# Optimization experiments

Hardware: AMD Instinct MI355X
Metric: run time of the kernel (lower is better)

Reference implementation:

```python
import jax, jax.numpy as jnp
import numpy as np

SEQ = 4096
EMB = 1024
OUT = 1024


def setup_inputs() -> dict:
    key = jax.random.key(0)
    k_x, k_q, k_k, k_v = jax.random.split(key, 4)
    scale = 1.0 / np.sqrt(EMB)
    inputs = jax.random.normal(k_x, (SEQ, EMB), dtype=jnp.float32)
    # torch Linear weight is (out_features, in_features); y = x @ W.T
    W_Q = jax.random.normal(k_q, (OUT, EMB), dtype=jnp.float32) * scale
    W_K = jax.random.normal(k_k, (OUT, EMB), dtype=jnp.float32) * scale
    W_V = jax.random.normal(k_v, (OUT, EMB), dtype=jnp.float32) * scale
    return {"inputs": inputs, "W_Q": W_Q, "W_K": W_K, "W_V": W_V}


def reference(inputs, W_Q, W_K, W_V):
    # projections: (S, E) @ (E, D) -> (S, D)
    q = inputs @ W_Q.T
    k = inputs @ W_K.T
    v = inputs @ W_V.T
    d_k = k.shape[-1]
    scores = (q @ k.T) / jnp.sqrt(jnp.asarray(d_k, dtype=q.dtype))  # (S, S)
    weights = jax.nn.softmax(scores, axis=-1)
    return weights @ v  # (S, D)
```

## Files before the change

kernel.cpp:

```cpp
#include <hip/hip_runtime.h>

typedef __bf16 bf16;
typedef __bf16 bf16x4 __attribute__((ext_vector_type(4)));
typedef __bf16 bf16x8 __attribute__((ext_vector_type(8)));
typedef float f32x4 __attribute__((ext_vector_type(4)));

#define SEQ 4096
#define EMB 1024

#define MODE_BF16 0
#define MODE_EXP  1
#define MODE_PART 2

__device__ __forceinline__ void async_copy16(void* lds, const void* g) {
    __builtin_amdgcn_global_load_lds(
        (const __attribute__((address_space(1))) unsigned int*)g,
        (__attribute__((address_space(3))) unsigned int*)lds,
        16, 0, 0);
}

__global__ __launch_bounds__(256) void cvt_f32_bf16(const float* __restrict__ src,
                                                    bf16* __restrict__ dst, int n)
{
    int i = (blockIdx.x * 256 + threadIdx.x) * 4;
    if (i < n) {
        float4 f = *(const float4*)(src + i);
        bf16x4 v = { (bf16)f.x, (bf16)f.y, (bf16)f.z, (bf16)f.w };
        *(bf16x4*)(dst + i) = v;
    }
}

template<int OUT_MODE>
__global__ __launch_bounds__(256) void gemm_bt(const bf16* __restrict__ A,
                                               const bf16* __restrict__ B,
                                               void* __restrict__ Cv,
                                               float* __restrict__ Cpart,
                                               int lda, int ldb, int ldc, int K)
{
    __shared__ __align__(16) bf16 As[128 * 64];
    __shared__ __align__(16) bf16 Bs[128 * 64];

    const int tid  = threadIdx.x;
    const int lane = tid & 63;
    const int wave = tid >> 6;
    const int m0 = blockIdx.y * 128;
    const int n0 = blockIdx.x * 128;
    const size_t koff = (size_t)blockIdx.z * K;

    const int srow = tid >> 3;
    const int spc  = tid & 7;
    const int sl   = (spc - (srow & 7)) & 7;

    const int wm = (wave & 1) << 6;
    const int wn = (wave >> 1) << 6;
    const int fr = lane & 15;
    const int q  = lane >> 4;

    f32x4 acc[4][4];
    for (int i = 0; i < 4; i++)
        for (int j = 0; j < 4; j++)
            acc[i][j] = {0.f, 0.f, 0.f, 0.f};

    const bf16* Ab = A + (size_t)(m0 + srow) * lda + koff + sl * 8;
    const bf16* Bb = B + (size_t)(n0 + srow) * ldb + koff + sl * 8;

    bf16* AsD = &As[srow * 64 + spc * 8];
    bf16* BsD = &Bs[srow * 64 + spc * 8];

    const int pc0 = ((q + fr) & 7) * 8;
    const int pc1 = (((q + fr) & 7) ^ 4) * 8;

    for (int k0 = 0; k0 < K; k0 += 64) {
        __syncthreads();
        for (int t = 0; t < 4; t++) {
            async_copy16(AsD + t * 2048, Ab + k0 + (size_t)(32 * t) * lda);
            async_copy16(BsD + t * 2048, Bb + k0 + (size_t)(32 * t) * ldb);
        }
        __syncthreads();

        bf16x8 af[4], bg[4];
        for (int i = 0; i < 4; i++)
            af[i] = *(const bf16x8*)&As[(wm + i * 16 + fr) * 64 + pc0];
        for (int j = 0; j < 4; j++)
            bg[j] = *(const bf16x8*)&Bs[(wn + j * 16 + fr) * 64 + pc0];
        for (int i = 0; i < 4; i++)
            for (int j = 0; j < 4; j++)
                acc[i][j] = __builtin_amdgcn_mfma_f32_16x16x32_bf16(af[i], bg[j], acc[i][j], 0, 0, 0);
        for (int i = 0; i < 4; i++)
            af[i] = *(const bf16x8*)&As[(wm + i * 16 + fr) * 64 + pc1];
        for (int j = 0; j < 4; j++)
            bg[j] = *(const bf16x8*)&Bs[(wn + j * 16 + fr) * 64 + pc1];
        for (int i = 0; i < 4; i++)
            for (int j = 0; j < 4; j++)
                acc[i][j] = __builtin_amdgcn_mfma_f32_16x16x32_bf16(af[i], bg[j], acc[i][j], 0, 0, 0);
    }

    const int cm = m0 + wm + (q << 2);
    const int cn = n0 + wn + fr;
    if (OUT_MODE == MODE_BF16) {
        bf16* C = (bf16*)Cv;
        for (int i = 0; i < 4; i++)
            for (int j = 0; j < 4; j++)
                for (int r = 0; r < 4; r++)
                    C[(size_t)(cm + i * 16 + r) * ldc + (cn + j * 16)] = (bf16)acc[i][j][r];
    } else if (OUT_MODE == MODE_EXP) {
        bf16* C = (bf16*)Cv;
        for (int i = 0; i < 4; i++)
            for (int j = 0; j < 4; j++)
                for (int r = 0; r < 4; r++)
                    C[(size_t)(cm + i * 16 + r) * ldc + (cn + j * 16)] =
                        (bf16)__expf(acc[i][j][r] * 0.03125f);
    } else {
        float* C = (blockIdx.z == 0) ? (float*)Cv
                                     : Cpart + (size_t)(blockIdx.z - 1) * SEQ * 1024;
        for (int i = 0; i < 4; i++)
            for (int j = 0; j < 4; j++)
                for (int r = 0; r < 4; r++)
                    C[(size_t)(cm + i * 16 + r) * ldc + (cn + j * 16)] = acc[i][j][r];
    }
}

__global__ __launch_bounds__(256) void reduce_norm(const bf16* __restrict__ E,
                                                   const float* __restrict__ p1,
                                                   const float* __restrict__ p2,
                                                   const float* __restrict__ p3,
                                                   float* __restrict__ out)
{
    const int m = blockIdx.x;
    const int tid = threadIdx.x;

    const bf16* er = E + (size_t)m * 4096;
    bf16x8 v0 = *(const bf16x8*)&er[tid * 16];
    bf16x8 v1 = *(const bf16x8*)&er[tid * 16 + 8];
    float s = 0.f;
    for (int i = 0; i < 8; i++) s += (float)v0[i] + (float)v1[i];
    for (int t = 1; t < 64; t <<= 1) s += __shfl_xor(s, t);

    __shared__ float red[4];
    if ((tid & 63) == 0) red[tid >> 6] = s;
    __syncthreads();
    const float inv = 1.f / (red[0] + red[1] + red[2] + red[3]);

    const size_t off = (size_t)m * 1024 + tid * 4;
    float4 a = *(const float4*)(out + off);
    float4 b = *(const float4*)(p1 + off);
    float4 c = *(const float4*)(p2 + off);
    float4 d = *(const float4*)(p3 + off);
    float4 o;
    o.x = (a.x + b.x + c.x + d.x) * inv;
    o.y = (a.y + b.y + c.y + d.y) * inv;
    o.z = (a.z + b.z + c.z + d.z) * inv;
    o.w = (a.w + b.w + c.w + d.w) * inv;
    *(float4*)(out + off) = o;
}

extern "C" void kernel_launch(void* const* d_in, const int* in_sizes, int n_in,
                              void* d_out, int out_size, void* d_ws, size_t ws_size,
                              hipStream_t stream)
{
    const float* x  = (const float*)d_in[0];
    const float* wq = (const float*)d_in[1];
    const float* wk = (const float*)d_in[2];
    const float* wv = (const float*)d_in[3];
    float* out = (float*)d_out;

    char* ws = (char*)d_ws;
    const size_t MB = 1024 * 1024;
    bf16*  E   = (bf16*)(ws);
    float* p1  = (float*)(ws + 32 * MB);
    float* p2  = (float*)(ws + 48 * MB);
    float* p3  = (float*)(ws + 64 * MB);
    bf16*  xb  = (bf16*)(ws + 32 * MB);
    bf16*  wqk = (bf16*)(ws + 40 * MB);
    bf16*  wvb = (bf16*)(ws + 44 * MB);
    bf16*  QK  = (bf16*)(ws + 64 * MB);
    bf16*  VT  = (bf16*)(ws + 80 * MB);

    dim3 blk(256);

    cvt_f32_bf16<<<dim3(SEQ * EMB / 1024), blk, 0, stream>>>(x,  xb, SEQ * EMB);
    cvt_f32_bf16<<<dim3(EMB * EMB / 1024), blk, 0, stream>>>(wq, wqk, EMB * EMB);
    cvt_f32_bf16<<<dim3(EMB * EMB / 1024), blk, 0, stream>>>(wk, wqk + EMB * EMB, EMB * EMB);
    cvt_f32_bf16<<<dim3(EMB * EMB / 1024), blk, 0, stream>>>(wv, wvb, EMB * EMB);

    gemm_bt<MODE_BF16><<<dim3(16, 32), blk, 0, stream>>>(xb, wqk, QK, nullptr,
                                                         1024, 1024, 2048, 1024);
    gemm_bt<MODE_BF16><<<dim3(32, 8), blk, 0, stream>>>(wvb, xb, VT, nullptr,
                                                        1024, 1024, 4096, 1024);
    gemm_bt<MODE_EXP><<<dim3(32, 32), blk, 0, stream>>>(QK, QK + 1024, E, nullptr,
                                                        2048, 2048, 4096, 1024);
    gemm_bt<MODE_PART><<<dim3(8, 32, 4), blk, 0, stream>>>(E, VT, out, p1,
                                                           4096, 4096, 1024, 1024);
    reduce_norm<<<dim3(SEQ), blk, 0, stream>>>(E, p1, p2, p3, out);
}
```

Before: 240.9 us.

## Fuse softmax row sums into exp GEMM and use atomic split-K accumulation

Merges the four conversion kernels into one prep kernel, which also zeroes the output and a row-sum buffer. The exp-scores GEMM now reduces row sums in registers and atomically adds them. The split-K PV GEMM atomically accumulates into the output instead of writing partial buffers. A light scale_rows kernel replaces the reduce kernel, so E is no longer re-read and three partial buffers are no longer written and read. The cost is many float atomics in the epilogue and a summation order that is no longer deterministic.

```diff
diff --git a/kernel.cpp b/kernel.cpp
--- a/kernel.cpp
+++ b/kernel.cpp
@@ -10,7 +10,7 @@
 
 #define MODE_BF16 0
 #define MODE_EXP  1
-#define MODE_PART 2
+#define MODE_ATOM 2
 
 __device__ __forceinline__ void async_copy16(void* lds, const void* g) {
     __builtin_amdgcn_global_load_lds(
@@ -19,22 +19,41 @@
         16, 0, 0);
 }
 
-__global__ __launch_bounds__(256) void cvt_f32_bf16(const float* __restrict__ src,
-                                                    bf16* __restrict__ dst, int n)
+__global__ __launch_bounds__(256) void prep_all(const float* __restrict__ x,
+                                                const float* __restrict__ wq,
+                                                const float* __restrict__ wk,
+                                                const float* __restrict__ wv,
+                                                bf16* __restrict__ xb,
+                                                bf16* __restrict__ wqk,
+                                                bf16* __restrict__ wvb,
+                                                float* __restrict__ out,
+                                                float* __restrict__ rowsum)
 {
-    int i = (blockIdx.x * 256 + threadIdx.x) * 4;
-    if (i < n) {
-        float4 f = *(const float4*)(src + i);
-        bf16x4 v = { (bf16)f.x, (bf16)f.y, (bf16)f.z, (bf16)f.w };
-        *(bf16x4*)(dst + i) = v;
+    const int u = blockIdx.x * 256 + threadIdx.x;
+    const float* src;
+    bf16* dst;
+    int off;
+    if (u < 1048576)      { src = x;  dst = xb;               off = u; }
+    else if (u < 1310720) { src = wq; dst = wqk;              off = u - 1048576; }
+    else if (u < 1572864) { src = wk; dst = wqk + EMB * EMB;  off = u - 1310720; }
+    else if (u < 1835008) { src = wv; dst = wvb;              off = u - 1572864; }
+    else if (u < 2883584) {
+        *(float4*)(out + (size_t)(u - 1835008) * 4) = float4{0.f, 0.f, 0.f, 0.f};
+        return;
+    } else {
+        *(float4*)(rowsum + (size_t)(u - 2883584) * 4) = float4{0.f, 0.f, 0.f, 0.f};
+        return;
     }
+    float4 f = *(const float4*)(src + (size_t)off * 4);
+    bf16x4 v = { (bf16)f.x, (bf16)f.y, (bf16)f.z, (bf16)f.w };
+    *(bf16x4*)(dst + (size_t)off * 4) = v;
 }
 
 template<int OUT_MODE>
 __global__ __launch_bounds__(256) void gemm_bt(const bf16* __restrict__ A,
                                                const bf16* __restrict__ B,
                                                void* __restrict__ Cv,
-                                               float* __restrict__ Cpart,
+                                               float* __restrict__ rowsum,
                                                int lda, int ldb, int ldc, int K)
 {
     __shared__ __align__(16) bf16 As[128 * 64];
@@ -105,53 +124,43 @@
                     C[(size_t)(cm + i * 16 + r) * ldc + (cn + j * 16)] = (bf16)acc[i][j][r];
     } else if (OUT_MODE == MODE_EXP) {
         bf16* C = (bf16*)Cv;
+        float rs[4][4];
+        for (int i = 0; i < 4; i++)
+            for (int r = 0; r < 4; r++) rs[i][r] = 0.f;
+        for (int i = 0; i < 4; i++)
+            for (int j = 0; j < 4; j++)
+                for (int r = 0; r < 4; r++) {
+                    float e = __expf(acc[i][j][r] * 0.03125f);
+                    C[(size_t)(cm + i * 16 + r) * ldc + (cn + j * 16)] = (bf16)e;
+                    rs[i][r] += e;
+                }
+        for (int i = 0; i < 4; i++)
+            for (int r = 0; r < 4; r++)
+                for (int m = 1; m < 16; m <<= 1)
+                    rs[i][r] += __shfl_xor(rs[i][r], m);
+        if (fr == 0)
+            for (int i = 0; i < 4; i++)
+                for (int r = 0; r < 4; r++)
+                    unsafeAtomicAdd(&rowsum[cm + i * 16 + r], rs[i][r]);
+    } else {
+        float* C = (float*)Cv;
         for (int i = 0; i < 4; i++)
             for (int j = 0; j < 4; j++)
                 for (int r = 0; r < 4; r++)
-                    C[(size_t)(cm + i * 16 + r) * ldc + (cn + j * 16)] =
-                        (bf16)__expf(acc[i][j][r] * 0.03125f);
-    } else {
-        float* C = (blockIdx.z == 0) ? (float*)Cv
-                                     : Cpart + (size_t)(blockIdx.z - 1) * SEQ * 1024;
-        for (int i = 0; i < 4; i++)
-            for (int j = 0; j < 4; j++)
-                for (int r = 0; r < 4; r++)
-                    C[(size_t)(cm + i * 16 + r) * ldc + (cn + j * 16)] = acc[i][j][r];
+                    unsafeAtomicAdd(&C[(size_t)(cm + i * 16 + r) * ldc + (cn + j * 16)],
+                                    acc[i][j][r]);
     }
 }
 
-__global__ __launch_bounds__(256) void reduce_norm(const bf16* __restrict__ E,
-                                                   const float* __restrict__ p1,
-                                                   const float* __restrict__ p2,
-                                                   const float* __restrict__ p3,
-                                                   float* __restrict__ out)
+__global__ __launch_bounds__(256) void scale_rows(float* __restrict__ out,
+                                                  const float* __restrict__ rowsum)
 {
-    const int m = blockIdx.x;
-    const int tid = threadIdx.x;
-
-    const bf16* er = E + (size_t)m * 4096;
-    bf16x8 v0 = *(const bf16x8*)&er[tid * 16];
-    bf16x8 v1 = *(const bf16x8*)&er[tid * 16 + 8];
-    float s = 0.f;
-    for (int i = 0; i < 8; i++) s += (float)v0[i] + (float)v1[i];
-    for (int t = 1; t < 64; t <<= 1) s += __shfl_xor(s, t);
-
-    __shared__ float red[4];
-    if ((tid & 63) == 0) red[tid >> 6] = s;
-    __syncthreads();
-    const float inv = 1.f / (red[0] + red[1] + red[2] + red[3]);
-
-    const size_t off = (size_t)m * 1024 + tid * 4;
-    float4 a = *(const float4*)(out + off);
-    float4 b = *(const float4*)(p1 + off);
-    float4 c = *(const float4*)(p2 + off);
-    float4 d = *(const float4*)(p3 + off);
-    float4 o;
-    o.x = (a.x + b.x + c.x + d.x) * inv;
-    o.y = (a.y + b.y + c.y + d.y) * inv;
-    o.z = (a.z + b.z + c.z + d.z) * inv;
-    o.w = (a.w + b.w + c.w + d.w) * inv;
-    *(float4*)(out + off) = o;
+    const int gid = blockIdx.x * 256 + threadIdx.x;
+    const int row = gid >> 8;
+    const float inv = 1.f / rowsum[row];
+    float4 v = *(const float4*)(out + (size_t)gid * 4);
+    v.x *= inv; v.y *= inv; v.z *= inv; v.w *= inv;
+    *(float4*)(out + (size_t)gid * 4) = v;
 }
 
 extern "C" void kernel_launch(void* const* d_in, const int* in_sizes, int n_in,
@@ -167,29 +176,24 @@
     char* ws = (char*)d_ws;
     const size_t MB = 1024 * 1024;
     bf16*  E   = (bf16*)(ws);
-    float* p1  = (float*)(ws + 32 * MB);
-    float* p2  = (float*)(ws + 48 * MB);
-    float* p3  = (float*)(ws + 64 * MB);
     bf16*  xb  = (bf16*)(ws + 32 * MB);
     bf16*  wqk = (bf16*)(ws + 40 * MB);
     bf16*  wvb = (bf16*)(ws + 44 * MB);
+    float* rsm = (float*)(ws + 46 * MB);
     bf16*  QK  = (bf16*)(ws + 64 * MB);
     bf16*  VT  = (bf16*)(ws + 80 * MB);
 
     dim3 blk(256);
 
-    cvt_f32_bf16<<<dim3(SEQ * EMB / 1024), blk, 0, stream>>>(x,  xb, SEQ * EMB);
-    cvt_f32_bf16<<<dim3(EMB * EMB / 1024), blk, 0, stream>>>(wq, wqk, EMB * EMB);
-    cvt_f32_bf16<<<dim3(EMB * EMB / 1024), blk, 0, stream>>>(wk, wqk + EMB * EMB, EMB * EMB);
-    cvt_f32_bf16<<<dim3(EMB * EMB / 1024), blk, 0, stream>>>(wv, wvb, EMB * EMB);
+    prep_all<<<dim3(11268), blk, 0, stream>>>(x, wq, wk, wv, xb, wqk, wvb, out, rsm);
 
     gemm_bt<MODE_BF16><<<dim3(16, 32), blk, 0, stream>>>(xb, wqk, QK, nullptr,
                                                          1024, 1024, 2048, 1024);
     gemm_bt<MODE_BF16><<<dim3(32, 8), blk, 0, stream>>>(wvb, xb, VT, nullptr,
                                                         1024, 1024, 4096, 1024);
-    gemm_bt<MODE_EXP><<<dim3(32, 32), blk, 0, stream>>>(QK, QK + 1024, E, nullptr,
+    gemm_bt<MODE_EXP><<<dim3(32, 32), blk, 0, stream>>>(QK, QK + 1024, E, rsm,
                                                         2048, 2048, 4096, 1024);
-    gemm_bt<MODE_PART><<<dim3(8, 32, 4), blk, 0, stream>>>(E, VT, out, p1,
+    gemm_bt<MODE_ATOM><<<dim3(8, 32, 4), blk, 0, stream>>>(E, VT, out, nullptr,
                                                            4096, 4096, 1024, 1024);
-    reduce_norm<<<dim3(SEQ), blk, 0, stream>>>(E, p1, p2, p3, out);
+    scale_rows<<<dim3(4096), blk, 0, stream>>>(out, rsm);
 }
```

New measurement: 276.5 us. 14.8% more time.
